# Kernel tuning notes

Hardware: AMD Instinct MI355X
Metric: run time of the kernel (lower is better)

Reference implementation:

```python
import jax, jax.numpy as jnp
import numpy as np

INFEATURES = 4096
OUTFEATURES = 11008
GROUP_SIZE = 128
N_GROUPS = INFEATURES // GROUP_SIZE  # 32
PACK = 8  # 32 bits / 4 bits


def _unpack_int4(packed):
    # packed: [R, C//8] int32 -> [R, C] int32 nibbles in [0, 15]
    shifts = (jnp.arange(PACK, dtype=jnp.int32) * 4)
    nib = (packed[:, :, None] >> shifts[None, None, :]) & 0xF
    return nib.reshape(packed.shape[0], packed.shape[1] * PACK)


def setup_inputs() -> dict:
    key = jax.random.key(0)
    k1, k2, k3, k4, k5 = jax.random.split(key, 5)
    x = jax.random.normal(k1, (2048, INFEATURES), dtype=jnp.float32)
    qweight = jax.random.randint(k2, (INFEATURES, OUTFEATURES // PACK), 0, 2147483647, dtype=jnp.int32)
    qzeros = jax.random.randint(k3, (N_GROUPS, OUTFEATURES // PACK), 0, 2147483647, dtype=jnp.int32)
    scales = jax.random.uniform(k4, (N_GROUPS, OUTFEATURES), minval=0.001, maxval=0.01, dtype=jnp.float32)
    bias = jax.random.normal(k5, (OUTFEATURES,), dtype=jnp.float32) * 0.01
    return {"x": x, "qweight": qweight, "qzeros": qzeros, "scales": scales, "bias": bias}


def reference(x, qweight, qzeros, scales, bias):
    # convert_from_uint4: dequantize packed int4 weight with per-group scale/zero
    w_int = _unpack_int4(qweight)                       # [in, out] int4 values
    z_int = _unpack_int4(qzeros)                        # [n_groups, out]
    dt = scales.dtype
    # broadcast group params to per-row (trivial g_idx: row i -> group i // GROUP_SIZE)
    z = jnp.repeat(z_int.astype(dt), GROUP_SIZE, axis=0)      # [in, out]
    s = jnp.repeat(scales, GROUP_SIZE, axis=0)                # [in, out]
    weight = (w_int.astype(dt) - z) * s                       # [in, out]
    out = jnp.matmul(x, weight) + bias                        # [tokens, out]
    return out
```

## Files before the change

### kernel.cpp

```cpp
#include <hip/hip_runtime.h>

typedef __bf16 bf16_t;
typedef bf16_t bf16x8 __attribute__((ext_vector_type(8)));
typedef float  floatx4 __attribute__((ext_vector_type(4)));
typedef unsigned int uint;

constexpr int Mdim = 2048;
constexpr int Kdim = 4096;
constexpr int Ndim = 11008;
constexpr int NPK  = Ndim / 8;
constexpr int BM = 128, BN = 128, BK = 64;
constexpr int SA = 72;
constexpr int SB = 72;
constexpr int SQ = 68;

__global__ void xcast_kernel(const float* __restrict__ x, bf16_t* __restrict__ xb)
{
    const int i = (blockIdx.x * 256 + threadIdx.x) * 8;
    const float4 a = *(const float4*)(x + i);
    const float4 b = *(const float4*)(x + i + 4);
    bf16x8 v;
    v[0] = (bf16_t)a.x; v[1] = (bf16_t)a.y; v[2] = (bf16_t)a.z; v[3] = (bf16_t)a.w;
    v[4] = (bf16_t)b.x; v[5] = (bf16_t)b.y; v[6] = (bf16_t)b.z; v[7] = (bf16_t)b.w;
    *(bf16x8*)(xb + i) = v;
}

template <bool PRE>
__global__ __launch_bounds__(256, 3)
void qgemm_kernel(const float* __restrict__ x,
                  const bf16_t* __restrict__ xb,
                  const uint* __restrict__ qweight,
                  const uint* __restrict__ qzeros,
                  const float* __restrict__ scales,
                  const float* __restrict__ bias,
                  float* __restrict__ out)
{
    __shared__ bf16_t As[BM * SA];
    __shared__ bf16_t Bs[BN * SB];
    __shared__ uint   qbuf[16 * SQ];

    const int t  = threadIdx.x;
    const int m0 = blockIdx.y * BM;
    const int n0 = blockIdx.x * BN;
    const int c0 = n0 >> 3;

    const int wave = t >> 6;
    const int lane = t & 63;
    const int quad = lane >> 4;
    const int l16  = lane & 15;
    const int mw = (wave >> 1) * 64;
    const int nw = (wave & 1) * 64;

    floatx4 acc[4][4];
#pragma unroll
    for (int i = 0; i < 4; ++i)
#pragma unroll
        for (int j = 0; j < 4; ++j)
            acc[i][j] = (floatx4){0.f, 0.f, 0.f, 0.f};

    const int am = t >> 3;
    const int ao = t & 7;
    const int qk  = t >> 2;
    const int qc4 = (t & 3) * 4;
    const int nloc  = t & 127;
    const int khalf = t >> 7;
    const int cc    = nloc >> 3;
    const int jsh   = (nloc & 7) * 4;

    for (int kt = 0; kt < Kdim / BK; ++kt) {
        const int k0 = kt * BK;
        const int g  = k0 >> 7;

#pragma unroll
        for (int p = 0; p < 4; ++p) {
            const int m = p * 32 + am;
            if (PRE) {
                const bf16x8 v = *(const bf16x8*)(xb + (size_t)(m0 + m) * Kdim + k0 + ao * 8);
                *(bf16x8*)&As[m * SA + ao * 8] = v;
            } else {
                const float* src = x + (size_t)(m0 + m) * Kdim + k0 + ao * 8;
                const float4 a = *(const float4*)src;
                const float4 b = *(const float4*)(src + 4);
                bf16x8 v;
                v[0] = (bf16_t)a.x; v[1] = (bf16_t)a.y; v[2] = (bf16_t)a.z; v[3] = (bf16_t)a.w;
                v[4] = (bf16_t)b.x; v[5] = (bf16_t)b.y; v[6] = (bf16_t)b.z; v[7] = (bf16_t)b.w;
                *(bf16x8*)&As[m * SA + ao * 8] = v;
            }
        }
        {
            const uint4 w4 = *(const uint4*)(qweight + (size_t)(k0 + qk) * NPK + c0 + qc4);
            qbuf[(qc4 + 0) * SQ + qk] = w4.x;
            qbuf[(qc4 + 1) * SQ + qk] = w4.y;
            qbuf[(qc4 + 2) * SQ + qk] = w4.z;
            qbuf[(qc4 + 3) * SQ + qk] = w4.w;
        }
        __syncthreads();

        {
            const uint  zw = qzeros[(size_t)g * NPK + c0 + cc];
            const float s  = scales[(size_t)g * Ndim + n0 + nloc];
            const float zs = (float)((zw >> jsh) & 15u) * s;
            const uint* qrow = &qbuf[cc * SQ + khalf * 32];
#pragma unroll
            for (int j = 0; j < 4; ++j) {
                const uint4 qa = *(const uint4*)(qrow + j * 8);
                const uint4 qb = *(const uint4*)(qrow + j * 8 + 4);
                bf16x8 v;
                v[0] = (bf16_t)((float)((qa.x >> jsh) & 15u) * s - zs);
                v[1] = (bf16_t)((float)((qa.y >> jsh) & 15u) * s - zs);
                v[2] = (bf16_t)((float)((qa.z >> jsh) & 15u) * s - zs);
                v[3] = (bf16_t)((float)((qa.w >> jsh) & 15u) * s - zs);
                v[4] = (bf16_t)((float)((qb.x >> jsh) & 15u) * s - zs);
                v[5] = (bf16_t)((float)((qb.y >> jsh) & 15u) * s - zs);
                v[6] = (bf16_t)((float)((qb.z >> jsh) & 15u) * s - zs);
                v[7] = (bf16_t)((float)((qb.w >> jsh) & 15u) * s - zs);
                *(bf16x8*)&Bs[nloc * SB + khalf * 32 + j * 8] = v;
            }
        }
        __syncthreads();

#pragma unroll
        for (int s = 0; s < 2; ++s) {
            bf16x8 fa[4], fb[4];
#pragma unroll
            for (int mt = 0; mt < 4; ++mt)
                fa[mt] = *(const bf16x8*)&As[(mw + mt * 16 + l16) * SA + s * 32 + quad * 8];
#pragma unroll
            for (int nt = 0; nt < 4; ++nt)
                fb[nt] = *(const bf16x8*)&Bs[(nw + nt * 16 + l16) * SB + s * 32 + quad * 8];
#pragma unroll
            for (int mt = 0; mt < 4; ++mt)
#pragma unroll
                for (int nt = 0; nt < 4; ++nt)
                    acc[mt][nt] = __builtin_amdgcn_mfma_f32_16x16x32_bf16(fa[mt], fb[nt], acc[mt][nt], 0, 0, 0);
        }
        __syncthreads();
    }

#pragma unroll
    for (int nt = 0; nt < 4; ++nt) {
        const int col = n0 + nw + nt * 16 + l16;
        const float b = bias[col];
#pragma unroll
        for (int mt = 0; mt < 4; ++mt) {
#pragma unroll
            for (int r = 0; r < 4; ++r) {
                const int row = m0 + mw + mt * 16 + quad * 4 + r;
                out[(size_t)row * Ndim + col] = acc[mt][nt][r] + b;
            }
        }
    }
}

extern "C" void kernel_launch(void* const* d_in, const int* in_sizes, int n_in,
                              void* d_out, int out_size, void* d_ws, size_t ws_size,
                              hipStream_t stream)
{
    const float* x        = (const float*)d_in[0];
    const uint*  qweight  = (const uint*)d_in[1];
    const uint*  qzeros   = (const uint*)d_in[2];
    const float* scales   = (const float*)d_in[3];
    const float* bias     = (const float*)d_in[4];
    float*       out      = (float*)d_out;
    bf16_t*      xb       = (bf16_t*)d_ws;

    const size_t xb_bytes = (size_t)Mdim * Kdim * sizeof(bf16_t);
    dim3 grid(Ndim / BN, Mdim / BM);

    if (ws_size >= xb_bytes) {
        xcast_kernel<<<(Mdim * Kdim) / (256 * 8), 256, 0, stream>>>(x, xb);
        qgemm_kernel<true><<<grid, dim3(256), 0, stream>>>(x, xb, qweight, qzeros, scales, bias, out);
    } else {
        qgemm_kernel<false><<<grid, dim3(256), 0, stream>>>(x, xb, qweight, qzeros, scales, bias, out);
    }
}
```

Baseline: 399.1 us.

## Pre-dequantize int4 weights to bf16 once, then run plain bf16 GEMM with direct-to-LDS loads

Adds a separate kernel that dequantizes the packed int4 weights into a transposed bf16 [N,K] workspace buffer once per call. The GEMM then reads the ready bf16 tiles with global_load_lds, which writes straight into LDS without passing through registers. This removes the per-tile dequantization that the fused kernel repeated for every M block and drops one barrier per K step. In exchange it adds about 90MB of workspace writes and reads plus an extra launch. The unpadded LDS stride may also cause bank conflicts on fragment reads. The new path runs only when the workspace is large enough.

```diff
diff --git a/kernel.cpp b/kernel.cpp
--- a/kernel.cpp
+++ b/kernel.cpp
@@ -14,6 +14,10 @@
 constexpr int SB = 72;
 constexpr int SQ = 68;
 
+#define GLOAD_LDS16(g, l) \
+    __builtin_amdgcn_global_load_lds((const __attribute__((address_space(1))) void*)(g), \
+                                     (__attribute__((address_space(3))) void*)(l), 16, 0, 0)
+
 __global__ void xcast_kernel(const float* __restrict__ x, bf16_t* __restrict__ xb)
 {
     const int i = (blockIdx.x * 256 + threadIdx.x) * 8;
@@ -23,6 +27,149 @@
     v[0] = (bf16_t)a.x; v[1] = (bf16_t)a.y; v[2] = (bf16_t)a.z; v[3] = (bf16_t)a.w;
     v[4] = (bf16_t)b.x; v[5] = (bf16_t)b.y; v[6] = (bf16_t)b.z; v[7] = (bf16_t)b.w;
     *(bf16x8*)(xb + i) = v;
+}
+
+__global__ __launch_bounds__(256, 4)
+void wdeq_kernel(const uint* __restrict__ qweight, const uint* __restrict__ qzeros,
+                 const float* __restrict__ scales, bf16_t* __restrict__ wt)
+{
+    __shared__ uint qbuf[16 * SQ];
+    const int t  = threadIdx.x;
+    const int n0 = blockIdx.x * 128;
+    const int k0 = blockIdx.y * 64;
+    const int c0 = n0 >> 3;
+    const int g  = k0 >> 7;
+
+    const int qk  = t >> 2;
+    const int qc4 = (t & 3) * 4;
+    const uint4 w4 = *(const uint4*)(qweight + (size_t)(k0 + qk) * NPK + c0 + qc4);
+    qbuf[(qc4 + 0) * SQ + qk] = w4.x;
+    qbuf[(qc4 + 1) * SQ + qk] = w4.y;
+    qbuf[(qc4 + 2) * SQ + qk] = w4.z;
+    qbuf[(qc4 + 3) * SQ + qk] = w4.w;
+    __syncthreads();
+
+    const int nloc  = t & 127;
+    const int khalf = t >> 7;
+    const int cc    = nloc >> 3;
+    const int jsh   = (nloc & 7) * 4;
+
+    const uint  zw = qzeros[(size_t)g * NPK + c0 + cc];
+    const float s  = scales[(size_t)g * Ndim + n0 + nloc];
+    const float zs = (float)((zw >> jsh) & 15u) * s;
+    const uint* qrow = &qbuf[cc * SQ + khalf * 32];
+    bf16_t* dst = wt + (size_t)(n0 + nloc) * Kdim + k0 + khalf * 32;
+#pragma unroll
+    for (int j = 0; j < 4; ++j) {
+        const uint4 qa = *(const uint4*)(qrow + j * 8);
+        const uint4 qb = *(const uint4*)(qrow + j * 8 + 4);
+        bf16x8 v;
+        v[0] = (bf16_t)((float)((qa.x >> jsh) & 15u) * s - zs);
+        v[1] = (bf16_t)((float)((qa.y >> jsh) & 15u) * s - zs);
+        v[2] = (bf16_t)((float)((qa.z >> jsh) & 15u) * s - zs);
+        v[3] = (bf16_t)((float)((qa.w >> jsh) & 15u) * s - zs);
+        v[4] = (bf16_t)((float)((qb.x >> jsh) & 15u) * s - zs);
+        v[5] = (bf16_t)((float)((qb.y >> jsh) & 15u) * s - zs);
+        v[6] = (bf16_t)((float)((qb.z >> jsh) & 15u) * s - zs);
+        v[7] = (bf16_t)((float)((qb.w >> jsh) & 15u) * s - zs);
+        *(bf16x8*)(dst + j * 8) = v;
+    }
+}
+
+template <bool PREX>
+__global__ __launch_bounds__(256, 4)
+void gemm_kernel(const float* __restrict__ x, const bf16_t* __restrict__ xb,
+                 const bf16_t* __restrict__ wt, const float* __restrict__ bias,
+                 float* __restrict__ out)
+{
+    constexpr int SAg = PREX ? 64 : 72;
+    __shared__ bf16_t As[128 * SAg];
+    __shared__ bf16_t Bs[128 * 64];
+
+    const int t    = threadIdx.x;
+    const int m0   = blockIdx.y * BM;
+    const int n0   = blockIdx.x * BN;
+    const int wave = t >> 6;
+    const int lane = t & 63;
+    const int quad = lane >> 4;
+    const int l16  = lane & 15;
+    const int mw = (wave >> 1) * 64;
+    const int nw = (wave & 1) * 64;
+
+    floatx4 acc[4][4];
+#pragma unroll
+    for (int i = 0; i < 4; ++i)
+#pragma unroll
+        for (int j = 0; j < 4; ++j)
+            acc[i][j] = (floatx4){0.f, 0.f, 0.f, 0.f};
+
+    const int am = t >> 3;
+    const int ao = t & 7;
+    const int lr = lane >> 3;
+    const int lo = (lane & 7) * 8;
+
+    for (int kt = 0; kt < Kdim / BK; ++kt) {
+        const int k0 = kt * BK;
+
+        if (PREX) {
+#pragma unroll
+            for (int p = 0; p < 4; ++p) {
+                const int q = wave * 4 + p;
+                GLOAD_LDS16(xb + (size_t)(m0 + q * 8 + lr) * Kdim + k0 + lo,
+                            As + q * 512);
+            }
+        } else {
+#pragma unroll
+            for (int p = 0; p < 4; ++p) {
+                const int m = p * 32 + am;
+                const float* src = x + (size_t)(m0 + m) * Kdim + k0 + ao * 8;
+                const float4 a = *(const float4*)src;
+                const float4 b = *(const float4*)(src + 4);
+                bf16x8 v;
+                v[0] = (bf16_t)a.x; v[1] = (bf16_t)a.y; v[2] = (bf16_t)a.z; v[3] = (bf16_t)a.w;
+                v[4] = (bf16_t)b.x; v[5] = (bf16_t)b.y; v[6] = (bf16_t)b.z; v[7] = (bf16_t)b.w;
+                *(bf16x8*)&As[m * SAg + ao * 8] = v;
+            }
+        }
+#pragma unroll
+        for (int p = 0; p < 4; ++p) {
+            const int q = wave * 4 + p;
+            GLOAD_LDS16(wt + (size_t)(n0 + q * 8 + lr) * Kdim + k0 + lo,
+                        Bs + q * 512);
+        }
+        __syncthreads();
+
+#pragma unroll
+        for (int s = 0; s < 2; ++s) {
+            bf16x8 fa[4], fb[4];
+#pragma unroll
+            for (int mt = 0; mt < 4; ++mt)
+                fa[mt] = *(const bf16x8*)&As[(mw + mt * 16 + l16) * SAg + s * 32 + quad * 8];
+#pragma unroll
+            for (int nt = 0; nt < 4; ++nt)
+                fb[nt] = *(const bf16x8*)&Bs[(nw + nt * 16 + l16) * 64 + s * 32 + quad * 8];
+#pragma unroll
+            for (int mt = 0; mt < 4; ++mt)
+#pragma unroll
+                for (int nt = 0; nt < 4; ++nt)
+                    acc[mt][nt] = __builtin_amdgcn_mfma_f32_16x16x32_bf16(fa[mt], fb[nt], acc[mt][nt], 0, 0, 0);
+        }
+        __syncthreads();
+    }
+
+#pragma unroll
+    for (int nt = 0; nt < 4; ++nt) {
+        const int col = n0 + nw + nt * 16 + l16;
+        const float b = bias[col];
+#pragma unroll
+        for (int mt = 0; mt < 4; ++mt) {
+#pragma unroll
+            for (int r = 0; r < 4; ++r) {
+                const int row = m0 + mw + mt * 16 + quad * 4 + r;
+                out[(size_t)row * Ndim + col] = acc[mt][nt][r] + b;
+            }
+        }
+    }
 }
 
 template <bool PRE>
@@ -162,15 +309,29 @@
     const float* scales   = (const float*)d_in[3];
     const float* bias     = (const float*)d_in[4];
     float*       out      = (float*)d_out;
-    bf16_t*      xb       = (bf16_t*)d_ws;
-
+
+    const size_t wb_bytes = (size_t)Kdim * Ndim * sizeof(bf16_t);
     const size_t xb_bytes = (size_t)Mdim * Kdim * sizeof(bf16_t);
-    dim3 grid(Ndim / BN, Mdim / BM);
-
-    if (ws_size >= xb_bytes) {
-        xcast_kernel<<<(Mdim * Kdim) / (256 * 8), 256, 0, stream>>>(x, xb);
-        qgemm_kernel<true><<<grid, dim3(256), 0, stream>>>(x, xb, qweight, qzeros, scales, bias, out);
+
+    dim3 ggrid(Ndim / BN, Mdim / BM);
+
+    if (ws_size >= wb_bytes) {
+        bf16_t* wt = (bf16_t*)d_ws;
+        wdeq_kernel<<<dim3(Ndim / 128, Kdim / 64), 256, 0, stream>>>(qweight, qzeros, scales, wt);
+        if (ws_size >= wb_bytes + xb_bytes) {
+            bf16_t* xb = (bf16_t*)((char*)d_ws + wb_bytes);
+            xcast_kernel<<<(Mdim * Kdim) / (256 * 8), 256, 0, stream>>>(x, xb);
+            gemm_kernel<true><<<ggrid, dim3(256), 0, stream>>>(x, xb, wt, bias, out);
+        } else {
+            gemm_kernel<false><<<ggrid, dim3(256), 0, stream>>>(x, nullptr, wt, bias, out);
+        }
     } else {
-        qgemm_kernel<false><<<grid, dim3(256), 0, stream>>>(x, xb, qweight, qzeros, scales, bias, out);
-    }
-}
+        bf16_t* xb = (bf16_t*)d_ws;
+        if (ws_size >= xb_bytes) {
+            xcast_kernel<<<(Mdim * Kdim) / (256 * 8), 256, 0, stream>>>(x, xb);
+            qgemm_kernel<true><<<ggrid, dim3(256), 0, stream>>>(x, xb, qweight, qzeros, scales, bias, out);
+        } else {
+            qgemm_kernel<false><<<ggrid, dim3(256), 0, stream>>>(x, xb, qweight, qzeros, scales, bias, out);
+        }
+    }
+}
```

Result: slower. 409.8 us (+2.7%).
